# Kernel optimization log

Hardware: AMD Instinct MI355X
Metric: run time of the kernel (lower is better)

The kernel has to match this reference:

```python
import jax, jax.numpy as jnp
import numpy as np
import math


def _instance_cl(z1, z2):
    # z1, z2: [B, T, C] -> per-element instance contrastive loss [B, T]
    B = z1.shape[0]
    z = jnp.concatenate([z1, z2], axis=0)          # [2B, T, C]
    z = z.transpose(1, 0, 2)                        # [T, 2B, C]
    sim = jnp.einsum('tic,tjc->tij', z, z)          # [T, 2B, 2B]
    # drop diagonal: tril(-1) shifted + triu(1) shifted -> [T, 2B, 2B-1]
    logits = jnp.tril(sim, -1)[:, :, :-1] + jnp.triu(sim, 1)[:, :, 1:]
    logits = -jax.nn.log_softmax(logits, axis=-1)
    i = jnp.arange(B)
    loss = (logits[:, i, B + i - 1] + logits[:, B + i, i]) / 2.0   # [T, B]
    return loss.T                                    # [B, T]


def _temporal_cl(z1, z2):
    # z1, z2: [B, T, C] -> per-timestep temporal contrastive loss [B, T]
    T = z1.shape[1]
    z = jnp.concatenate([z1, z2], axis=1)            # [B, 2T, C]
    sim = jnp.einsum('bic,bjc->bij', z, z)           # [B, 2T, 2T]
    logits = jnp.tril(sim, -1)[:, :, :-1] + jnp.triu(sim, 1)[:, :, 1:]
    logits = -jax.nn.log_softmax(logits, axis=-1)
    t = jnp.arange(T)
    return (logits[:, t, T + t - 1] + logits[:, T + t, t]) / 2.0   # [B, T]


def _contrastive_corr(z1, z2, alpha=0.5):
    # per-(batch, timestep) contrastive score, shape [B, L]
    return alpha * _instance_cl(z1, z2) + (1.0 - alpha) * _temporal_cl(z1, z2)


def setup_inputs() -> dict:
    key = jax.random.key(0)
    k1, k2, k3 = jax.random.split(key, 3)
    B, L, H, E = 4, 2048, 8, 64
    queries = jax.random.normal(k1, (B, L, H, E), dtype=jnp.float32)
    keys = jax.random.normal(k2, (B, L, H, E), dtype=jnp.float32)
    values = jax.random.normal(k3, (B, L, H, E), dtype=jnp.float32)
    attn_mask = jnp.zeros((1,), dtype=bool)  # unused; ProbMask is rebuilt internally
    return {"queries": queries, "keys": keys, "values": values, "attn_mask": attn_mask}


FACTOR = 1.0


def reference(queries, keys, values, attn_mask):
    B, L, H, E = queries.shape
    # S == L here so key/value slicing branch is a no-op
    corr = _contrastive_corr(queries.reshape(B, L, H * E),
                             keys.reshape(B, L, H * E))       # [B, L]
    top_k = int(FACTOR * math.log(L))                          # static (=7 for L=2048)
    _, index = jax.lax.top_k(corr.mean(axis=0), top_k)         # [K]
    corr_top = corr[:, index]                                  # [B, K]
    # scores[b,h,k,l] = corr_top[b,k] broadcast over h and l
    scores = jnp.broadcast_to(corr_top[:, None, :, None], (B, H, top_k, L))
    # ProbMask: mask future positions l > index[k] (causal for the selected queries)
    mask = jnp.arange(L)[None, :] > index[:, None]             # [K, L]
    scores = jnp.where(mask[None, None, :, :], -jnp.inf, scores)
    attn = jax.nn.softmax(scores, axis=-1)                     # [B, H, K, L]
    V = values.transpose(0, 2, 1, 3)                           # [B, H, L, D]
    context = jnp.cumsum(V, axis=2)                            # initial context (mask_flag=True)
    out = jnp.einsum('bhkl,bhld->bhkd', attn, V)               # [B, H, K, D]
    context = context.at[:, :, index, :].set(out)              # scatter update
    return context
```

## Files before the change

kernel.cpp:

```cpp
#include <hip/hip_runtime.h>
#include <math.h>


typedef __attribute__((ext_vector_type(8))) short short8;
typedef __attribute__((ext_vector_type(8))) unsigned short ushort8;
typedef __attribute__((ext_vector_type(4))) float f32x4;

typedef const __attribute__((address_space(1))) void* gas_ptr;
typedef __attribute__((address_space(3))) void* las_ptr;

#define EXP_OFF 80.0f

__device__ __forceinline__ void async_cp16(const void* g, void* l) {
  __builtin_amdgcn_global_load_lds((gas_ptr)g, (las_ptr)l, 16, 0, 0);
}

__device__ __forceinline__ unsigned short f2bf(float x) {
  union { float f; unsigned int u; } v; v.f = x;
  unsigned int r = v.u + 0x7FFFu + ((v.u >> 16) & 1u);
  return (unsigned short)(r >> 16);
}

__global__ __launch_bounds__(256) void convert_bf16_kernel(
    const float* __restrict__ Q, const float* __restrict__ K,
    unsigned short* __restrict__ Z) {
  int tid = blockIdx.x * 256 + threadIdx.x;
  int row = tid >> 6;
  int c0 = (tid & 63) * 8;
  int b = row >> 12, i = row & 4095;
  const float* src = (i < 2048)
      ? Q + ((size_t)(b * 2048 + i) * 512 + c0)
      : K + ((size_t)(b * 2048 + (i - 2048)) * 512 + c0);
  float4 v0 = ((const float4*)src)[0];
  float4 v1 = ((const float4*)src)[1];
  ushort8 o;
  o[0] = f2bf(v0.x); o[1] = f2bf(v0.y); o[2] = f2bf(v0.z); o[3] = f2bf(v0.w);
  o[4] = f2bf(v1.x); o[5] = f2bf(v1.y); o[6] = f2bf(v1.z); o[7] = f2bf(v1.w);
  *(ushort8*)(Z + (size_t)row * 512 + c0) = o;
}

__global__ __launch_bounds__(256, 3) void temporal_gemm_kernel(
    const unsigned short* __restrict__ Z, float* __restrict__ part,
    float* __restrict__ lse_inst ,
    float* __restrict__ posdot ) {
  __shared__ __align__(16) unsigned short As[3][128 * 32];
  __shared__ __align__(16) unsigned short Bs[3][128 * 32];

  if (blockIdx.x >= 2112) {
    int wave = ((blockIdx.x - 2112) * 256 + threadIdx.x) >> 6;
    int t0 = wave * 2;
    int lane = threadIdx.x & 63;
    int lm = lane & 15, q = lane >> 4;
    int tt = (lm < 8) ? t0 : t0 + 1;
    int v = lm & 7;
    size_t zrow = (v < 4) ? ((size_t)v * 4096 + tt)
                          : ((size_t)(v - 4) * 4096 + 2048 + tt);
    const unsigned short* g = Z + zrow * 512 + q * 8;

    f32x4 acc0 = (f32x4)(0.f), acc1 = (f32x4)(0.f);
#pragma unroll
    for (int kc = 0; kc < 16; kc += 2) {
      short8 a0 = *(const short8*)(g + kc * 32);
      short8 a1 = *(const short8*)(g + kc * 32 + 32);
      acc0 = __builtin_amdgcn_mfma_f32_16x16x32_bf16(a0, a0, acc0, 0, 0, 0);
      acc1 = __builtin_amdgcn_mfma_f32_16x16x32_bf16(a1, a1, acc1, 0, 0, 0);
    }
    f32x4 acc = acc0 + acc1;

#pragma unroll
    for (int rr = 0; rr < 4; rr++) {
      int i = q * 4 + rr;
      float val = acc[rr];
      bool samehalf = ((i < 8) == (lm < 8));
      int t = (i < 8) ? t0 : t0 + 1;
      int iv = i & 7;
      if (samehalf && iv < 4 && (lm & 7) == iv + 4)
        posdot[iv * 2048 + t] = val;
      float dd = (samehalf && lm != i) ? val : -INFINITY;
      float mt = dd;
      mt = fmaxf(mt, __shfl_xor(mt, 1));
      mt = fmaxf(mt, __shfl_xor(mt, 2));
      mt = fmaxf(mt, __shfl_xor(mt, 4));
      float e = __expf(dd - mt);
      e += __shfl_xor(e, 1);
      e += __shfl_xor(e, 2);
      e += __shfl_xor(e, 4);
      if ((lm & 7) == 0 && samehalf) lse_inst[t * 8 + iv] = mt + __logf(e);
    }
    return;
  }

  int id = blockIdx.x;
  int x = id & 7;
  int b = x >> 1;
  int t = (id >> 3) * 2 + (x & 1);
  int cj = (int)((sqrtf(8.0f * (float)t + 1.0f) - 1.0f) * 0.5f);
  while ((cj + 1) * (cj + 2) / 2 <= t) cj++;
  while (cj * (cj + 1) / 2 > t) cj--;
  int ri = t - cj * (cj + 1) / 2;
  const unsigned short* Zb = Z + (size_t)b * 4096 * 512;

  int tid = threadIdx.x;
  int w = tid >> 6, lane = tid & 63;
  int wr = w >> 1, wc = w & 1;
  int lm = lane & 15, q = lane >> 4;
  int swz = q ^ ((lm >> 1) & 3);

  int srow = lane >> 2;
  int kq = (lane & 3) ^ ((lane >> 3) & 3);
  int rl0 = w * 16 + srow;
  int rl1 = 64 + rl0;
  const unsigned short* gA0 = Zb + (size_t)(ri * 128 + rl0) * 512 + kq * 8;
  const unsigned short* gA1 = Zb + (size_t)(ri * 128 + rl1) * 512 + kq * 8;
  const unsigned short* gB0 = Zb + (size_t)(cj * 128 + rl0) * 512 + kq * 8;
  const unsigned short* gB1 = Zb + (size_t)(cj * 128 + rl1) * 512 + kq * 8;
  int lo0 = (w * 16) * 32;
  int lo1 = (64 + w * 16) * 32;

  f32x4 acc[4][4];
#pragma unroll
  for (int mi = 0; mi < 4; mi++)
#pragma unroll
    for (int ni = 0; ni < 4; ni++) acc[mi][ni] = (f32x4)(0.f);

#define STAGE(kc_, sl_)                                  \
  do {                                                   \
    int go_ = (kc_) * 32;                                \
    async_cp16(gA0 + go_, As[sl_] + lo0);                \
    async_cp16(gA1 + go_, As[sl_] + lo1);                \
    async_cp16(gB0 + go_, Bs[sl_] + lo0);                \
    async_cp16(gB1 + go_, Bs[sl_] + lo1);                \
  } while (0)

  STAGE(0, 0);
  STAGE(1, 1);

  int sl = 0;
  for (int kc = 0; kc < 16; ++kc) {
    if (kc < 15)
      asm volatile("s_waitcnt vmcnt(4)" ::: "memory");
    else
      asm volatile("s_waitcnt vmcnt(0)" ::: "memory");
    asm volatile("s_barrier" ::: "memory");

    if (kc + 2 < 16) {
      int ss = sl + 2;
      if (ss >= 3) ss -= 3;
      STAGE(kc + 2, ss);
    }

    short8 af[4], bfr[4];
#pragma unroll
    for (int mi = 0; mi < 4; mi++) {
      int ar = wr * 64 + mi * 16 + lm;
      af[mi] = *(const short8*)(As[sl] + ar * 32 + swz * 8);
    }
#pragma unroll
    for (int ni = 0; ni < 4; ni++) {
      int bc = wc * 64 + ni * 16 + lm;
      bfr[ni] = *(const short8*)(Bs[sl] + bc * 32 + swz * 8);
    }
#pragma unroll
    for (int mi = 0; mi < 4; mi++)
#pragma unroll
      for (int ni = 0; ni < 4; ni++)
        acc[mi][ni] = __builtin_amdgcn_mfma_f32_16x16x32_bf16(
            af[mi], bfr[ni], acc[mi][ni], 0, 0, 0);

    sl = (sl + 1 == 3) ? 0 : sl + 1;
  }
#undef STAGE

  float rsum[4][4];
  float csum[4];
#pragma unroll
  for (int mi = 0; mi < 4; mi++)
#pragma unroll
    for (int rr = 0; rr < 4; rr++) rsum[mi][rr] = 0.f;
#pragma unroll
  for (int ni = 0; ni < 4; ni++) csum[ni] = 0.f;

#pragma unroll
  for (int mi = 0; mi < 4; mi++) {
#pragma unroll
    for (int ni = 0; ni < 4; ni++) {
#pragma unroll
      for (int rr = 0; rr < 4; rr++) {
        int R = ri * 128 + wr * 64 + mi * 16 + q * 4 + rr;
        int Cg = cj * 128 + wc * 64 + ni * 16 + lm;
        float e = (R != Cg) ? __expf(acc[mi][ni][rr] - EXP_OFF) : 0.f;
        rsum[mi][rr] += e;
        csum[ni] += e;
      }
    }
  }

#pragma unroll
  for (int mi = 0; mi < 4; mi++) {
#pragma unroll
    for (int rr = 0; rr < 4; rr++) {
      float s = rsum[mi][rr];
      s += __shfl_xor(s, 1);
      s += __shfl_xor(s, 2);
      s += __shfl_xor(s, 4);
      s += __shfl_xor(s, 8);
      if (lm == 0) {
        int R = ri * 128 + wr * 64 + mi * 16 + q * 4 + rr;
        part[((size_t)(b * 4096 + R)) * 64 + cj * 2 + wc] = s;
      }
    }
  }

  if (ri != cj) {
#pragma unroll
    for (int ni = 0; ni < 4; ni++) {
      float s = csum[ni];
      s += __shfl_xor(s, 16);
      s += __shfl_xor(s, 32);
      if (q == 0) {
        int Cg = cj * 128 + wc * 64 + ni * 16 + lm;
        part[((size_t)(b * 4096 + Cg)) * 64 + ri * 2 + wr] = s;
      }
    }
  }
}

__global__ __launch_bounds__(256) void merge_row_kernel(
    const float* __restrict__ part, float* __restrict__ lse_temp) {
  int row = blockIdx.x * 256 + threadIdx.x;
  const float4* p = (const float4*)(part + (size_t)row * 64);
  float s = 0.f;
#pragma unroll
  for (int i = 0; i < 16; i++) {
    float4 v = p[i];
    s += v.x + v.y + v.z + v.w;
  }
  lse_temp[row] = EXP_OFF + __logf(s);
}

__global__ __launch_bounds__(256) void combine_psum_kernel(
    const float* __restrict__ lse_inst, const float* __restrict__ lse_temp,
    const float* __restrict__ posdot, int* __restrict__ index_out,
    const float* __restrict__ V, float* __restrict__ psum) {
  if (blockIdx.x > 0) {
    int gb = (blockIdx.x - 1) * 4 + (threadIdx.x >> 6);
    int bh = gb >> 6, g = gb & 63;
    int h = bh & 7, b = bh >> 3;
    int lane = threadIdx.x & 63;
    int ro = lane >> 4, e4 = (lane & 15) * 4;
    const float* base =
        V + (size_t)(b * 2048 + g * 32 + ro) * 512 + h * 64 + e4;
    float sx = 0.f, sy = 0.f, sz = 0.f, sw = 0.f;
#pragma unroll
    for (int k = 0; k < 8; k++) {
      float4 v = *(const float4*)(base + (size_t)(k * 4) * 512);
      sx += v.x; sy += v.y; sz += v.z; sw += v.w;
    }
    sx += __shfl_xor(sx, 16); sy += __shfl_xor(sy, 16);
    sz += __shfl_xor(sz, 16); sw += __shfl_xor(sw, 16);
    sx += __shfl_xor(sx, 32); sy += __shfl_xor(sy, 32);
    sz += __shfl_xor(sz, 32); sw += __shfl_xor(sw, 32);
    if (ro == 0) {
      float4 o = {sx, sy, sz, sw};
      *(float4*)(psum + ((size_t)bh * 64 + g) * 64 + e4) = o;
    }
    return;
  }

  __shared__ float wmax[4];
  __shared__ int widx[4];
  int tid = threadIdx.x;
  int base = tid * 8;
  float v[8];
#pragma unroll
  for (int r = 0; r < 8; r++) {
    int t = base + r;
    float sum = 0.f;
#pragma unroll
    for (int b = 0; b < 4; b++) {
      sum += 0.25f * (lse_inst[t * 8 + b] + lse_inst[t * 8 + 4 + b] +
                      lse_temp[b * 4096 + t] + lse_temp[b * 4096 + 2048 + t]) -
             posdot[b * 2048 + t];
    }
    v[r] = sum * 0.25f;
  }
  int lane = tid & 63, w = tid >> 6;
  for (int k = 0; k < 7; k++) {
    float bv = v[0];
    int bi = base;
#pragma unroll
    for (int r = 1; r < 8; r++)
      if (v[r] > bv) { bv = v[r]; bi = base + r; }
#pragma unroll
    for (int d = 1; d < 64; d <<= 1) {
      float ov = __shfl_xor(bv, d);
      int oi = __shfl_xor(bi, d);
      if (ov > bv || (ov == bv && oi < bi)) { bv = ov; bi = oi; }
    }
    if (lane == 0) { wmax[w] = bv; widx[w] = bi; }
    __syncthreads();
    float BV = wmax[0];
    int BI = widx[0];
#pragma unroll
    for (int ww = 1; ww < 4; ww++)
      if (wmax[ww] > BV || (wmax[ww] == BV && widx[ww] < BI)) {
        BV = wmax[ww];
        BI = widx[ww];
      }
    if (tid == 0) index_out[k] = BI;
    if (BI >= base && BI < base + 8) v[BI - base] = -INFINITY;
    __syncthreads();
  }
}

__global__ __launch_bounds__(256) void cumsum_write_kernel(
    const float* __restrict__ V, const float* __restrict__ psum,
    const int* __restrict__ index, float* __restrict__ out) {
  int blk = blockIdx.x;
  int bh = blk >> 4, chunk = blk & 15;
  int h = bh & 7, b = bh >> 3;
  int tid = threadIdx.x;
  int e = tid & 63, sub = tid >> 6;
  int g = chunk * 4 + sub;

  const float* ps = psum + (size_t)bh * 64 * 64;
  float run = 0.f;
  for (int gg = 0; gg < g; ++gg) run += ps[gg * 64 + e];

  int idx[7];
#pragma unroll
  for (int k = 0; k < 7; k++) idx[k] = index[k];

  const float* Vbase = V + (size_t)(b * 2048) * 512 + h * 64 + e;
  float* obase = out + (size_t)bh * 2048 * 64 + e;

  int l0 = g * 32;
#pragma unroll 4
  for (int l = l0; l < l0 + 32; ++l) {
    run += Vbase[(size_t)l * 512];
    float o = run;
    bool special = false;
#pragma unroll
    for (int k = 0; k < 7; k++) special = special || (idx[k] == l);
    if (special) o = run / (float)(l + 1);
    obase[(size_t)l * 64] = o;
  }
}

extern "C" void kernel_launch(void* const* d_in, const int* in_sizes, int n_in,
                              void* d_out, int out_size, void* d_ws, size_t ws_size,
                              hipStream_t stream) {
  const float* Q = (const float*)d_in[0];
  const float* K = (const float*)d_in[1];
  const float* V = (const float*)d_in[2];
  float* out = (float*)d_out;

  unsigned short* Z = (unsigned short*)d_ws;
  float* base = (float*)d_ws + 4 * 4096 * 512 / 2;
  float* part = base;
  float* lse_t = base + 4 * 4096 * 64;
  float* lse_i = lse_t + 16384;
  float* posd = lse_i + 16384;
  int* idx = (int*)(posd + 8192);
  float* psum = part;

  convert_bf16_kernel<<<4096, 256, 0, stream>>>(Q, K, Z);
  temporal_gemm_kernel<<<2368, 256, 0, stream>>>(Z, part, lse_i, posd);
  merge_row_kernel<<<64, 256, 0, stream>>>(part, lse_t);
  combine_psum_kernel<<<513, 256, 0, stream>>>(lse_i, lse_t, posd, idx, V,
                                               psum);
  cumsum_write_kernel<<<512, 256, 0, stream>>>(V, psum, idx, out);
}
```

Before: 182.8 us.

## Fuse pipeline into three kernels with atomic row sums and redundant top-k

Moves the V block-sum work into the bf16 conversion launch and zeroes a row-sum buffer there. The GEMM now atomically adds its partial row and column exp-sums into that buffer instead of writing 64 partials per row. The separate merge kernel goes away, and the top-k selection is recomputed by every block of the cumsum kernel, which removes two launches and the index round-trip through memory. The costs are atomic contention in the GEMM epilogue, a non-deterministic summation order, and 512 blocks each redoing the 2048-element top-k with the log computations.

New measurement: 187.2 us. 1.02x slower.

```diff
diff --git a/kernel.cpp b/kernel.cpp
--- a/kernel.cpp
+++ b/kernel.cpp
@@ -21,10 +21,37 @@
   return (unsigned short)(r >> 16);
 }
 
-__global__ __launch_bounds__(256) void convert_bf16_kernel(
+__global__ __launch_bounds__(256) void convert_psum_kernel(
     const float* __restrict__ Q, const float* __restrict__ K,
-    unsigned short* __restrict__ Z) {
+    unsigned short* __restrict__ Z, float* __restrict__ sums,
+    const float* __restrict__ V, float* __restrict__ psum) {
+  if (blockIdx.x >= 4096) {
+    int gb = (blockIdx.x - 4096) * 4 + (threadIdx.x >> 6);
+    int bh = gb >> 6, g = gb & 63;
+    int h = bh & 7, b = bh >> 3;
+    int lane = threadIdx.x & 63;
+    int ro = lane >> 4, e4 = (lane & 15) * 4;
+    const float* base =
+        V + (size_t)(b * 2048 + g * 32 + ro) * 512 + h * 64 + e4;
+    float sx = 0.f, sy = 0.f, sz = 0.f, sw = 0.f;
+#pragma unroll
+    for (int k = 0; k < 8; k++) {
+      float4 v = *(const float4*)(base + (size_t)(k * 4) * 512);
+      sx += v.x; sy += v.y; sz += v.z; sw += v.w;
+    }
+    sx += __shfl_xor(sx, 16); sy += __shfl_xor(sy, 16);
+    sz += __shfl_xor(sz, 16); sw += __shfl_xor(sw, 16);
+    sx += __shfl_xor(sx, 32); sy += __shfl_xor(sy, 32);
+    sz += __shfl_xor(sz, 32); sw += __shfl_xor(sw, 32);
+    if (ro == 0) {
+      float4 o = {sx, sy, sz, sw};
+      *(float4*)(psum + ((size_t)bh * 64 + g) * 64 + e4) = o;
+    }
+    return;
+  }
+
   int tid = blockIdx.x * 256 + threadIdx.x;
+  if (tid < 16384) sums[tid] = 0.f;
   int row = tid >> 6;
   int c0 = (tid & 63) * 8;
   int b = row >> 12, i = row & 4095;
@@ -40,7 +67,7 @@
 }
 
 __global__ __launch_bounds__(256, 3) void temporal_gemm_kernel(
-    const unsigned short* __restrict__ Z, float* __restrict__ part,
+    const unsigned short* __restrict__ Z, float* __restrict__ sums,
     float* __restrict__ lse_inst ,
     float* __restrict__ posdot ) {
   __shared__ __align__(16) unsigned short As[3][128 * 32];
@@ -206,7 +233,7 @@
       s += __shfl_xor(s, 8);
       if (lm == 0) {
         int R = ri * 128 + wr * 64 + mi * 16 + q * 4 + rr;
-        part[((size_t)(b * 4096 + R)) * 64 + cj * 2 + wc] = s;
+        atomicAdd(&sums[b * 4096 + R], s);
       }
     }
   }
@@ -219,57 +246,20 @@
       s += __shfl_xor(s, 32);
       if (q == 0) {
         int Cg = cj * 128 + wc * 64 + ni * 16 + lm;
-        part[((size_t)(b * 4096 + Cg)) * 64 + ri * 2 + wr] = s;
+        atomicAdd(&sums[b * 4096 + Cg], s);
       }
     }
   }
 }
 
-__global__ __launch_bounds__(256) void merge_row_kernel(
-    const float* __restrict__ part, float* __restrict__ lse_temp) {
-  int row = blockIdx.x * 256 + threadIdx.x;
-  const float4* p = (const float4*)(part + (size_t)row * 64);
-  float s = 0.f;
-#pragma unroll
-  for (int i = 0; i < 16; i++) {
-    float4 v = p[i];
-    s += v.x + v.y + v.z + v.w;
-  }
-  lse_temp[row] = EXP_OFF + __logf(s);
-}
-
-__global__ __launch_bounds__(256) void combine_psum_kernel(
-    const float* __restrict__ lse_inst, const float* __restrict__ lse_temp,
-    const float* __restrict__ posdot, int* __restrict__ index_out,
-    const float* __restrict__ V, float* __restrict__ psum) {
-  if (blockIdx.x > 0) {
-    int gb = (blockIdx.x - 1) * 4 + (threadIdx.x >> 6);
-    int bh = gb >> 6, g = gb & 63;
-    int h = bh & 7, b = bh >> 3;
-    int lane = threadIdx.x & 63;
-    int ro = lane >> 4, e4 = (lane & 15) * 4;
-    const float* base =
-        V + (size_t)(b * 2048 + g * 32 + ro) * 512 + h * 64 + e4;
-    float sx = 0.f, sy = 0.f, sz = 0.f, sw = 0.f;
-#pragma unroll
-    for (int k = 0; k < 8; k++) {
-      float4 v = *(const float4*)(base + (size_t)(k * 4) * 512);
-      sx += v.x; sy += v.y; sz += v.z; sw += v.w;
-    }
-    sx += __shfl_xor(sx, 16); sy += __shfl_xor(sy, 16);
-    sz += __shfl_xor(sz, 16); sw += __shfl_xor(sw, 16);
-    sx += __shfl_xor(sx, 32); sy += __shfl_xor(sy, 32);
-    sz += __shfl_xor(sz, 32); sw += __shfl_xor(sw, 32);
-    if (ro == 0) {
-      float4 o = {sx, sy, sz, sw};
-      *(float4*)(psum + ((size_t)bh * 64 + g) * 64 + e4) = o;
-    }
-    return;
-  }
-
+__global__ __launch_bounds__(256) void cumsum_write_kernel(
+    const float* __restrict__ V, const float* __restrict__ psum,
+    const float* __restrict__ lse_inst, const float* __restrict__ sums,
+    const float* __restrict__ posdot, float* __restrict__ out) {
   __shared__ float wmax[4];
   __shared__ int widx[4];
   int tid = threadIdx.x;
+
   int base = tid * 8;
   float v[8];
 #pragma unroll
@@ -278,13 +268,16 @@
     float sum = 0.f;
 #pragma unroll
     for (int b = 0; b < 4; b++) {
+      float lt0 = EXP_OFF + __logf(sums[b * 4096 + t]);
+      float lt1 = EXP_OFF + __logf(sums[b * 4096 + 2048 + t]);
       sum += 0.25f * (lse_inst[t * 8 + b] + lse_inst[t * 8 + 4 + b] +
-                      lse_temp[b * 4096 + t] + lse_temp[b * 4096 + 2048 + t]) -
+                      lt0 + lt1) -
              posdot[b * 2048 + t];
     }
     v[r] = sum * 0.25f;
   }
   int lane = tid & 63, w = tid >> 6;
+  int idx[7];
   for (int k = 0; k < 7; k++) {
     float bv = v[0];
     int bi = base;
@@ -307,29 +300,20 @@
         BV = wmax[ww];
         BI = widx[ww];
       }
-    if (tid == 0) index_out[k] = BI;
+    idx[k] = BI;
     if (BI >= base && BI < base + 8) v[BI - base] = -INFINITY;
     __syncthreads();
   }
-}
-
-__global__ __launch_bounds__(256) void cumsum_write_kernel(
-    const float* __restrict__ V, const float* __restrict__ psum,
-    const int* __restrict__ index, float* __restrict__ out) {
+
   int blk = blockIdx.x;
   int bh = blk >> 4, chunk = blk & 15;
   int h = bh & 7, b = bh >> 3;
-  int tid = threadIdx.x;
   int e = tid & 63, sub = tid >> 6;
   int g = chunk * 4 + sub;
 
   const float* ps = psum + (size_t)bh * 64 * 64;
   float run = 0.f;
   for (int gg = 0; gg < g; ++gg) run += ps[gg * 64 + e];
-
-  int idx[7];
-#pragma unroll
-  for (int k = 0; k < 7; k++) idx[k] = index[k];
 
   const float* Vbase = V + (size_t)(b * 2048) * 512 + h * 64 + e;
   float* obase = out + (size_t)bh * 2048 * 64 + e;
@@ -357,17 +341,13 @@
 
   unsigned short* Z = (unsigned short*)d_ws;
   float* base = (float*)d_ws + 4 * 4096 * 512 / 2;
-  float* part = base;
-  float* lse_t = base + 4 * 4096 * 64;
-  float* lse_i = lse_t + 16384;
+  float* sums = base;
+  float* psum = base + 16384;
+  float* lse_i = psum + 131072;
   float* posd = lse_i + 16384;
-  int* idx = (int*)(posd + 8192);
-  float* psum = part;
-
-  convert_bf16_kernel<<<4096, 256, 0, stream>>>(Q, K, Z);
-  temporal_gemm_kernel<<<2368, 256, 0, stream>>>(Z, part, lse_i, posd);
-  merge_row_kernel<<<64, 256, 0, stream>>>(part, lse_t);
-  combine_psum_kernel<<<513, 256, 0, stream>>>(lse_i, lse_t, posd, idx, V,
-                                               psum);
-  cumsum_write_kernel<<<512, 256, 0, stream>>>(V, psum, idx, out);
-}
+
+  convert_psum_kernel<<<4608, 256, 0, stream>>>(Q, K, Z, sums, V, psum);
+  temporal_gemm_kernel<<<2368, 256, 0, stream>>>(Z, sums, lse_i, posd);
+  cumsum_write_kernel<<<512, 256, 0, stream>>>(V, psum, lse_i, sums, posd,
+                                               out);
+}
```

## Overlap V cumsum with contrastive GEMM and patch top-k rows afterwards

Applied to the files above, without the earlier changes.

The V block-sum pass moves into the bf16 conversion launch as extra blocks. The full cumsum write moves into the GEMM launch as extra blocks, so both run alongside the contrastive-loss work instead of after top-k selection. A small fixup kernel then rewrites only the 7 selected rows with the averaged value. psum gets its own workspace region because it no longer aliases part. This removes the serial dependency of the large output write on top-k and merges launches, at the cost of heavier, mixed-role grids that may disturb GEMM occupancy.

Measured after the change: 201.7 us. +10.4%, slower.

```diff
diff --git a/kernel.cpp b/kernel.cpp
--- a/kernel.cpp
+++ b/kernel.cpp
@@ -21,9 +21,35 @@
   return (unsigned short)(r >> 16);
 }
 
-__global__ __launch_bounds__(256) void convert_bf16_kernel(
+__global__ __launch_bounds__(256) void convert_psum_kernel(
     const float* __restrict__ Q, const float* __restrict__ K,
-    unsigned short* __restrict__ Z) {
+    unsigned short* __restrict__ Z, const float* __restrict__ V,
+    float* __restrict__ psum) {
+  if (blockIdx.x >= 4096) {
+    int gb = (blockIdx.x - 4096) * 4 + (threadIdx.x >> 6);
+    int bh = gb >> 6, g = gb & 63;
+    int h = bh & 7, b = bh >> 3;
+    int lane = threadIdx.x & 63;
+    int ro = lane >> 4, e4 = (lane & 15) * 4;
+    const float* base =
+        V + (size_t)(b * 2048 + g * 32 + ro) * 512 + h * 64 + e4;
+    float sx = 0.f, sy = 0.f, sz = 0.f, sw = 0.f;
+#pragma unroll
+    for (int k = 0; k < 8; k++) {
+      float4 v = *(const float4*)(base + (size_t)(k * 4) * 512);
+      sx += v.x; sy += v.y; sz += v.z; sw += v.w;
+    }
+    sx += __shfl_xor(sx, 16); sy += __shfl_xor(sy, 16);
+    sz += __shfl_xor(sz, 16); sw += __shfl_xor(sw, 16);
+    sx += __shfl_xor(sx, 32); sy += __shfl_xor(sy, 32);
+    sz += __shfl_xor(sz, 32); sw += __shfl_xor(sw, 32);
+    if (ro == 0) {
+      float4 o = {sx, sy, sz, sw};
+      *(float4*)(psum + ((size_t)bh * 64 + g) * 64 + e4) = o;
+    }
+    return;
+  }
+
   int tid = blockIdx.x * 256 + threadIdx.x;
   int row = tid >> 6;
   int c0 = (tid & 63) * 8;
@@ -42,9 +68,35 @@
 __global__ __launch_bounds__(256, 3) void temporal_gemm_kernel(
     const unsigned short* __restrict__ Z, float* __restrict__ part,
     float* __restrict__ lse_inst ,
-    float* __restrict__ posdot ) {
+    float* __restrict__ posdot ,
+    const float* __restrict__ V, const float* __restrict__ psum,
+    float* __restrict__ out) {
   __shared__ __align__(16) unsigned short As[3][128 * 32];
   __shared__ __align__(16) unsigned short Bs[3][128 * 32];
+
+  if (blockIdx.x >= 2368) {
+    int w2 = blockIdx.x - 2368;
+    int bh = w2 >> 4, chunk = w2 & 15;
+    int h = bh & 7, b = bh >> 3;
+    int tid = threadIdx.x;
+    int e = tid & 63, sub = tid >> 6;
+    int g = chunk * 4 + sub;
+
+    const float* ps = psum + (size_t)bh * 64 * 64;
+    float run = 0.f;
+    for (int gg = 0; gg < g; ++gg) run += ps[gg * 64 + e];
+
+    const float* Vbase = V + (size_t)(b * 2048) * 512 + h * 64 + e;
+    float* obase = out + (size_t)bh * 2048 * 64 + e;
+
+    int l0 = g * 32;
+#pragma unroll 4
+    for (int l = l0; l < l0 + 32; ++l) {
+      run += Vbase[(size_t)l * 512];
+      obase[(size_t)l * 64] = run;
+    }
+    return;
+  }
 
   if (blockIdx.x >= 2112) {
     int wave = ((blockIdx.x - 2112) * 256 + threadIdx.x) >> 6;
@@ -238,35 +290,9 @@
   lse_temp[row] = EXP_OFF + __logf(s);
 }
 
-__global__ __launch_bounds__(256) void combine_psum_kernel(
+__global__ __launch_bounds__(256) void combine_topk_kernel(
     const float* __restrict__ lse_inst, const float* __restrict__ lse_temp,
-    const float* __restrict__ posdot, int* __restrict__ index_out,
-    const float* __restrict__ V, float* __restrict__ psum) {
-  if (blockIdx.x > 0) {
-    int gb = (blockIdx.x - 1) * 4 + (threadIdx.x >> 6);
-    int bh = gb >> 6, g = gb & 63;
-    int h = bh & 7, b = bh >> 3;
-    int lane = threadIdx.x & 63;
-    int ro = lane >> 4, e4 = (lane & 15) * 4;
-    const float* base =
-        V + (size_t)(b * 2048 + g * 32 + ro) * 512 + h * 64 + e4;
-    float sx = 0.f, sy = 0.f, sz = 0.f, sw = 0.f;
-#pragma unroll
-    for (int k = 0; k < 8; k++) {
-      float4 v = *(const float4*)(base + (size_t)(k * 4) * 512);
-      sx += v.x; sy += v.y; sz += v.z; sw += v.w;
-    }
-    sx += __shfl_xor(sx, 16); sy += __shfl_xor(sy, 16);
-    sz += __shfl_xor(sz, 16); sw += __shfl_xor(sw, 16);
-    sx += __shfl_xor(sx, 32); sy += __shfl_xor(sy, 32);
-    sz += __shfl_xor(sz, 32); sw += __shfl_xor(sw, 32);
-    if (ro == 0) {
-      float4 o = {sx, sy, sz, sw};
-      *(float4*)(psum + ((size_t)bh * 64 + g) * 64 + e4) = o;
-    }
-    return;
-  }
-
+    const float* __restrict__ posdot, int* __restrict__ index_out) {
   __shared__ float wmax[4];
   __shared__ int widx[4];
   int tid = threadIdx.x;
@@ -313,37 +339,25 @@
   }
 }
 
-__global__ __launch_bounds__(256) void cumsum_write_kernel(
+__global__ __launch_bounds__(256) void fixup_kernel(
     const float* __restrict__ V, const float* __restrict__ psum,
     const int* __restrict__ index, float* __restrict__ out) {
-  int blk = blockIdx.x;
-  int bh = blk >> 4, chunk = blk & 15;
+  int bh = blockIdx.x;
   int h = bh & 7, b = bh >> 3;
   int tid = threadIdx.x;
-  int e = tid & 63, sub = tid >> 6;
-  int g = chunk * 4 + sub;
+  int e = tid & 63, w = tid >> 6;
 
   const float* ps = psum + (size_t)bh * 64 * 64;
-  float run = 0.f;
-  for (int gg = 0; gg < g; ++gg) run += ps[gg * 64 + e];
-
-  int idx[7];
-#pragma unroll
-  for (int k = 0; k < 7; k++) idx[k] = index[k];
-
   const float* Vbase = V + (size_t)(b * 2048) * 512 + h * 64 + e;
   float* obase = out + (size_t)bh * 2048 * 64 + e;
 
-  int l0 = g * 32;
-#pragma unroll 4
-  for (int l = l0; l < l0 + 32; ++l) {
-    run += Vbase[(size_t)l * 512];
-    float o = run;
-    bool special = false;
-#pragma unroll
-    for (int k = 0; k < 7; k++) special = special || (idx[k] == l);
-    if (special) o = run / (float)(l + 1);
-    obase[(size_t)l * 64] = o;
+  for (int k = w; k < 7; k += 4) {
+    int l = index[k];
+    int g = l >> 5;
+    float run = 0.f;
+    for (int gg = 0; gg < g; ++gg) run += ps[gg * 64 + e];
+    for (int ll = g * 32; ll <= l; ++ll) run += Vbase[(size_t)ll * 512];
+    obase[(size_t)l * 64] = run / (float)(l + 1);
   }
 }
 
@@ -358,16 +372,16 @@
   unsigned short* Z = (unsigned short*)d_ws;
   float* base = (float*)d_ws + 4 * 4096 * 512 / 2;
   float* part = base;
-  float* lse_t = base + 4 * 4096 * 64;
+  float* lse_t = part + 1048576;
   float* lse_i = lse_t + 16384;
   float* posd = lse_i + 16384;
-  int* idx = (int*)(posd + 8192);
-  float* psum = part;
-
-  convert_bf16_kernel<<<4096, 256, 0, stream>>>(Q, K, Z);
-  temporal_gemm_kernel<<<2368, 256, 0, stream>>>(Z, part, lse_i, posd);
+  float* psum = posd + 8192;
+  int* idx = (int*)(psum + 131072);
+
+  convert_psum_kernel<<<4608, 256, 0, stream>>>(Q, K, Z, V, psum);
+  temporal_gemm_kernel<<<2880, 256, 0, stream>>>(Z, part, lse_i, posd, V,
+                                                 psum, out);
   merge_row_kernel<<<64, 256, 0, stream>>>(part, lse_t);
-  combine_psum_kernel<<<513, 256, 0, stream>>>(lse_i, lse_t, posd, idx, V,
-                                               psum);
-  cumsum_write_kernel<<<512, 256, 0, stream>>>(V, psum, idx, out);
-}
+  combine_topk_kernel<<<1, 256, 0, stream>>>(lse_i, lse_t, posd, idx);
+  fixup_kernel<<<32, 256, 0, stream>>>(V, psum, idx, out);
+}
```
